# Kernel optimization log

Measured on AMD Instinct MI355X. Metric: run time of the kernel, lower is better.

## Reference

```python
import jax, jax.numpy as jnp
import numpy as np

EMBED_DIM = 1024
NUM_HEADS = 16
HEAD_DIM = EMBED_DIM // NUM_HEADS


def setup_inputs() -> dict:
    key = jax.random.key(0)
    k1, k2, k3, k4, k5 = jax.random.split(key, 5)
    B, S, D = 1, 4096, EMBED_DIM
    scale = 0.02
    return {
        "input": jax.random.normal(k1, (B, S, D), dtype=jnp.float32),
        "Wqkv": jax.random.normal(k2, (D, 3 * D), dtype=jnp.float32) * scale,
        "bqkv": jax.random.normal(k3, (3 * D,), dtype=jnp.float32) * scale,
        "Wo": jax.random.normal(k4, (D, D), dtype=jnp.float32) * scale,
        "bo": jax.random.normal(k5, (D,), dtype=jnp.float32) * scale,
    }


def reference(input, Wqkv, bqkv, Wo, bo):
    B, S, D = input.shape
    H, Hd = NUM_HEADS, HEAD_DIM
    qkv = input @ Wqkv + bqkv                        # [B, S, 3D]
    qkv = qkv.reshape(B, S, 3, H, Hd)
    qkv = jnp.transpose(qkv, (2, 0, 3, 1, 4))        # [3, B, H, S, Hd]
    q, k, v = qkv[0], qkv[1], qkv[2]
    scores = jnp.einsum("bhsd,bhtd->bhst", q, k) / (Hd ** 0.5)  # [B,H,S,S]
    causal = jnp.tril(jnp.ones((S, S), dtype=bool))[None, None]
    scores = jnp.where(causal, scores, -jnp.inf)
    attn = jax.nn.softmax(scores, axis=-1)
    out = jnp.einsum("bhst,bhtd->bhsd", attn, v)     # [B,H,S,Hd]
    out = jnp.transpose(out, (0, 2, 1, 3)).reshape(B, S, D)
    return out @ Wo + bo
```

## Files before the change

### kernel.cpp

```cpp
#include <hip/hip_runtime.h>

typedef __bf16 bf16;
typedef __bf16 bf16x8 __attribute__((ext_vector_type(8)));
typedef float f32x4 __attribute__((ext_vector_type(4)));
typedef float f32x16 __attribute__((ext_vector_type(16)));
typedef unsigned u32x2 __attribute__((ext_vector_type(2)));

#define MFMA16(a, b, c) __builtin_amdgcn_mfma_f32_16x16x32_bf16((a), (b), (c), 0, 0, 0)
#define MFMA32(a, b, c) __builtin_amdgcn_mfma_f32_32x32x16_bf16((a), (b), (c), 0, 0, 0)

typedef const __attribute__((address_space(1))) uint32_t glb_u32;
typedef __attribute__((address_space(3))) uint32_t lds_u32;
#define GLOAD16(gp, lp) __builtin_amdgcn_global_load_lds((glb_u32*)(gp), (lds_u32*)(lp), 16, 0, 0)

__global__ __launch_bounds__(256) void k_convX(const float* __restrict__ in, bf16* __restrict__ out) {
    size_t i = ((size_t)blockIdx.x * 256 + threadIdx.x) * 8;
    float4 a = *(const float4*)(in + i);
    float4 b = *(const float4*)(in + i + 4);
    bf16 e[8];
    e[0] = (bf16)a.x; e[1] = (bf16)a.y; e[2] = (bf16)a.z; e[3] = (bf16)a.w;
    e[4] = (bf16)b.x; e[5] = (bf16)b.y; e[6] = (bf16)b.z; e[7] = (bf16)b.w;
    uint4 u; __builtin_memcpy(&u, e, 16);
    *(uint4*)(out + i) = u;
}

__global__ __launch_bounds__(256) void k_tconv(const float* __restrict__ in, bf16* __restrict__ out,
                                               int R, int C) {
    __shared__ float tile[64][65];
    int bx = blockIdx.x, by = blockIdx.y;
    int t = threadIdx.x;
    for (int i = 0; i < 16; ++i) {
        int e = i * 256 + t; int r = e >> 6, c = e & 63;
        tile[r][c] = in[(size_t)(by * 64 + r) * C + bx * 64 + c];
    }
    __syncthreads();
    for (int i = 0; i < 16; ++i) {
        int e = i * 256 + t; int r = e >> 6, c = e & 63;
        out[(size_t)(bx * 64 + r) * R + by * 64 + c] = (bf16)tile[c][r];
    }
}

__device__ __forceinline__ void gemm128_core(const bf16* __restrict__ A, const bf16* __restrict__ Bt,
                                             int r0, int c0, int Kd, char* As, char* Bs,
                                             f32x4 (&acc)[4][4]) {
    int t = threadIdx.x, l = t & 63, w = t >> 6;
    int g = l >> 4, li = l & 15;
    int wr = w >> 1, wc = w & 1;
    for (int k0 = 0; k0 < Kd; k0 += 64) {
        __syncthreads();
        #pragma unroll
        for (int i = 0; i < 4; ++i) {
            int slot = i * 256 + t;
            int row = slot >> 3;
            int ch  = (slot & 7) ^ (row & 7);
            int base = (i * 256 + w * 64) * 16;
            GLOAD16(A  + (size_t)(r0 + row) * Kd + k0 + ch * 8, As + base);
            GLOAD16(Bt + (size_t)(c0 + row) * Kd + k0 + ch * 8, Bs + base);
        }
        __syncthreads();
        __builtin_amdgcn_s_setprio(1);
        #pragma unroll
        for (int kk = 0; kk < 2; ++kk) {
            bf16x8 af[4], bfr[4];
            #pragma unroll
            for (int m = 0; m < 4; ++m) {
                int row = wr * 64 + m * 16 + li;
                af[m] = *(const bf16x8*)(As + ((row * 128 + kk * 64 + g * 16) ^ ((row & 7) << 4)));
            }
            #pragma unroll
            for (int n = 0; n < 4; ++n) {
                int row = wc * 64 + n * 16 + li;
                bfr[n] = *(const bf16x8*)(Bs + ((row * 128 + kk * 64 + g * 16) ^ ((row & 7) << 4)));
            }
            #pragma unroll
            for (int m = 0; m < 4; ++m)
                #pragma unroll
                for (int n = 0; n < 4; ++n)
                    acc[m][n] = MFMA16(af[m], bfr[n], acc[m][n]);
        }
        __builtin_amdgcn_s_setprio(0);
    }
}

__global__ __launch_bounds__(256) void k_gemm_qkv(const bf16* __restrict__ Xb, const bf16* __restrict__ WqkvT,
                                                  const float* __restrict__ bqkv,
                                                  bf16* __restrict__ Q, bf16* __restrict__ Kfr,
                                                  bf16* __restrict__ Vfr) {
    __shared__ __align__(16) char As[16384];
    __shared__ __align__(16) char Bs[16384];
    int r0 = blockIdx.y * 128, c0 = blockIdx.x * 128;
    f32x4 acc[4][4] = {};
    gemm128_core(Xb, WqkvT, r0, c0, 1024, As, Bs, acc);
    int t = threadIdx.x, l = t & 63, w = t >> 6;
    int g = l >> 4, li = l & 15;
    int wr = w >> 1, wc = w & 1;
    int colbase = c0 + wc * 64;
    int sec = colbase >> 10;
    int head = (colbase & 1023) >> 6;
    if (sec == 0) {
        const float scale = 0.125f * 1.44269504f;
        #pragma unroll
        for (int m = 0; m < 4; ++m)
            #pragma unroll
            for (int n = 0; n < 4; ++n) {
                int hd = n * 16 + li;
                float bias = bqkv[colbase + hd];
                #pragma unroll
                for (int r = 0; r < 4; ++r) {
                    int row = r0 + wr * 64 + m * 16 + g * 4 + r;
                    Q[(size_t)(head * 4096 + row) * 64 + hd] = (bf16)((acc[m][n][r] + bias) * scale);
                }
            }
    } else if (sec == 1) {
        bf16* dstK = Kfr + (size_t)head * 262144;
        #pragma unroll
        for (int m = 0; m < 4; ++m) {
            int tbase = r0 + wr * 64 + m * 16 + g * 4;
            size_t tpart = (size_t)(tbase >> 5) * 2048 + (size_t)(tbase & 31) * 8;
            #pragma unroll
            for (int n = 0; n < 4; ++n) {
                int hd = n * 16 + li;
                float bias = bqkv[colbase + hd];
                size_t A0 = tpart + (size_t)(hd >> 4) * 512 + (size_t)((hd >> 3) & 1) * 256 + (hd & 7);
                #pragma unroll
                for (int r = 0; r < 4; ++r)
                    dstK[A0 + (size_t)r * 8] = (bf16)(acc[m][n][r] + bias);
            }
        }
    } else {
        bf16* dstV = Vfr + (size_t)head * 262144;
        #pragma unroll
        for (int m = 0; m < 4; ++m) {
            int tbase = r0 + wr * 64 + m * 16 + g * 4;
            size_t tpart = (size_t)(tbase >> 5) * 2048 + (size_t)((tbase >> 4) & 1) * 512
                         + (size_t)((tbase >> 3) & 1) * 256 + (tbase & 7);
            #pragma unroll
            for (int n = 0; n < 4; ++n) {
                int hd = n * 16 + li;
                float bias = bqkv[colbase + hd];
                size_t A0 = tpart + (size_t)(hd >> 5) * 1024 + (size_t)(hd & 31) * 8;
                bf16 e4[4];
                #pragma unroll
                for (int r = 0; r < 4; ++r) e4[r] = (bf16)(acc[m][n][r] + bias);
                unsigned long long pk; __builtin_memcpy(&pk, e4, 8);
                *(unsigned long long*)(dstV + A0) = pk;
            }
        }
    }
}

__global__ __launch_bounds__(256) void k_gemm_out(const bf16* __restrict__ Ob, const bf16* __restrict__ WoT,
                                                  const float* __restrict__ bo, float* __restrict__ out) {
    __shared__ __align__(16) char As[16384];
    __shared__ __align__(16) char Bs[8192];
    int r0 = blockIdx.y * 128, c0 = blockIdx.x * 64;
    int t = threadIdx.x, l = t & 63, w = t >> 6;
    int g = l >> 4, li = l & 15;
    f32x4 acc[2][4] = {};
    for (int k0 = 0; k0 < 1024; k0 += 64) {
        __syncthreads();
        #pragma unroll
        for (int i = 0; i < 4; ++i) {
            int slot = i * 256 + t;
            int row = slot >> 3;
            int ch  = (slot & 7) ^ (row & 7);
            int base = (i * 256 + w * 64) * 16;
            GLOAD16(Ob + (size_t)(r0 + row) * 1024 + k0 + ch * 8, As + base);
        }
        #pragma unroll
        for (int i = 0; i < 2; ++i) {
            int slot = i * 256 + t;
            int row = slot >> 3;
            int ch  = (slot & 7) ^ (row & 7);
            int base = (i * 256 + w * 64) * 16;
            GLOAD16(WoT + (size_t)(c0 + row) * 1024 + k0 + ch * 8, Bs + base);
        }
        __syncthreads();
        __builtin_amdgcn_s_setprio(1);
        #pragma unroll
        for (int kk = 0; kk < 2; ++kk) {
            bf16x8 af[2], bfr[4];
            #pragma unroll
            for (int m = 0; m < 2; ++m) {
                int row = w * 32 + m * 16 + li;
                af[m] = *(const bf16x8*)(As + ((row * 128 + kk * 64 + g * 16) ^ ((row & 7) << 4)));
            }
            #pragma unroll
            for (int n = 0; n < 4; ++n) {
                int row = n * 16 + li;
                bfr[n] = *(const bf16x8*)(Bs + ((row * 128 + kk * 64 + g * 16) ^ ((row & 7) << 4)));
            }
            #pragma unroll
            for (int m = 0; m < 2; ++m)
                #pragma unroll
                for (int n = 0; n < 4; ++n)
                    acc[m][n] = MFMA16(af[m], bfr[n], acc[m][n]);
        }
        __builtin_amdgcn_s_setprio(0);
    }
    #pragma unroll
    for (int m = 0; m < 2; ++m)
        #pragma unroll
        for (int n = 0; n < 4; ++n) {
            int col = c0 + n * 16 + li;
            float bias = bo[col];
            #pragma unroll
            for (int r = 0; r < 4; ++r) {
                int row = r0 + w * 32 + m * 16 + g * 4 + r;
                out[(size_t)row * 1024 + col] = acc[m][n][r] + bias;
            }
        }
}

__device__ __forceinline__ unsigned pkbf(float a, float b) {
    bf16 h0 = (bf16)a, h1 = (bf16)b;
    unsigned short u0, u1;
    __builtin_memcpy(&u0, &h0, 2); __builtin_memcpy(&u1, &h1, 2);
    return (unsigned)u0 | ((unsigned)u1 << 16);
}

__global__ __launch_bounds__(128) void k_attn(const bf16* __restrict__ Q, const uint4* __restrict__ Kfr,
                                              const uint4* __restrict__ Vfr, bf16* __restrict__ O) {
    __shared__ float Op[32][64];
    __shared__ float Ml[2][32];
    int bid = blockIdx.x;
    int h = bid & 15;
    int u = bid >> 4;
    int jj = (u < 64) ? u : 191 - u;
    int w = threadIdx.x >> 6;
    int l = threadIdx.x & 63;
    int lc = l & 31, hi = l >> 5;
    int hi4 = hi * 4, hi8 = hi * 8;
    const bf16* Qh = Q + (size_t)h * 4096 * 64;
    const uint4* Kh = Kfr + (size_t)h * 32768;
    const uint4* Vh = Vfr + (size_t)h * 32768;
    int nt = jj + 1;
    int hA = (nt + 1) >> 1;
    int tb = w ? hA : 0;
    int te = w ? nt : hA;

    f32x16 oacc[2] = {};
    float m = -1e30f, lsum = 0.f;
    uint4 kA[4], vA[4], kB[4], vB[4];
    bf16x8 qf[4];
    #pragma unroll
    for (int kst = 0; kst < 4; ++kst)
        qf[kst] = *(const bf16x8*)(Qh + (size_t)(jj * 32 + lc) * 64 + kst * 16 + hi8);

    auto compute = [&](int tt, uint4 (&kf)[4], uint4 (&vf)[4]) {
        f32x16 sacc = {};
        __builtin_amdgcn_s_setprio(1);
        #pragma unroll
        for (int kst = 0; kst < 4; ++kst) {
            bf16x8 kk; __builtin_memcpy(&kk, &kf[kst], 16);
            sacc = MFMA32(kk, qf[kst], sacc);
        }
        __builtin_amdgcn_s_setprio(0);
        if (tt == jj) {
            #pragma unroll
            for (int r = 0; r < 16; ++r) {
                int tloc = (r & 3) + 8 * (r >> 2) + hi4;
                if (tloc > lc) sacc[r] = -1e30f;
            }
        }
        float t8[8];
        #pragma unroll
        for (int r = 0; r < 8; ++r) t8[r] = fmaxf(sacc[r], sacc[r + 8]);
        float ta = fmaxf(fmaxf(t8[0], t8[1]), t8[2]);
        float tb3 = fmaxf(fmaxf(t8[3], t8[4]), t8[5]);
        float tc = fmaxf(t8[6], t8[7]);
        float pm = fmaxf(fmaxf(ta, tb3), tc);
        pm = fmaxf(pm, __shfl_xor(pm, 32));
        if (!__all(pm - m <= 8.0f)) {
            float mn = fmaxf(m, pm);
            float al = exp2f(m - mn);
            #pragma unroll
            for (int r = 0; r < 16; ++r) {
                int ql = (r & 3) + 8 * (r >> 2) + hi4;
                float alb = __shfl(al, ql);
                oacc[0][r] *= alb;
                oacc[1][r] *= alb;
            }
            lsum *= al;
            m = mn;
        }
        float pv[16];
        float rs0 = 0.f, rs1 = 0.f;
        #pragma unroll
        for (int r = 0; r < 8; ++r) {
            pv[r]     = exp2f(sacc[r] - m);     rs0 += pv[r];
            pv[r + 8] = exp2f(sacc[r + 8] - m); rs1 += pv[r + 8];
        }
        lsum += rs0 + rs1;
        #pragma unroll
        for (int ks = 0; ks < 2; ++ks) {
            int b = ks * 8;
            unsigned a0 = pkbf(pv[b + 0], pv[b + 1]), a1 = pkbf(pv[b + 2], pv[b + 3]);
            unsigned b0 = pkbf(pv[b + 4], pv[b + 5]), b1 = pkbf(pv[b + 6], pv[b + 7]);
            u32x2 r0 = __builtin_amdgcn_permlane32_swap(a0, b0, false, false);
            u32x2 r1 = __builtin_amdgcn_permlane32_swap(a1, b1, false, false);
            unsigned wsq[4] = { r0[0], r1[0], r0[1], r1[1] };
            bf16x8 pa; __builtin_memcpy(&pa, wsq, 16);
            __builtin_amdgcn_s_setprio(1);
            #pragma unroll
            for (int jt = 0; jt < 2; ++jt) {
                bf16x8 vv; __builtin_memcpy(&vv, &vf[jt * 2 + ks], 16);
                oacc[jt] = MFMA32(pa, vv, oacc[jt]);
            }
            __builtin_amdgcn_s_setprio(0);
        }
    };

    if (te > tb) {
        #pragma unroll
        for (int i = 0; i < 4; ++i) {
            kA[i] = Kh[(size_t)tb * 256 + i * 64 + l];
            vA[i] = Vh[(size_t)tb * 256 + i * 64 + l];
        }
        int i = tb;
        for (; i + 2 <= te; i += 2) {
            const uint4* Kn = Kh + (size_t)(i + 1) * 256;
            const uint4* Vn = Vh + (size_t)(i + 1) * 256;
            #pragma unroll
            for (int q = 0; q < 4; ++q) { kB[q] = Kn[q * 64 + l]; vB[q] = Vn[q * 64 + l]; }
            compute(i, kA, vA);
            if (i + 2 < te) {
                const uint4* K2 = Kh + (size_t)(i + 2) * 256;
                const uint4* V2 = Vh + (size_t)(i + 2) * 256;
                #pragma unroll
                for (int q = 0; q < 4; ++q) { kA[q] = K2[q * 64 + l]; vA[q] = V2[q * 64 + l]; }
            }
            compute(i + 1, kB, vB);
        }
        if ((te - tb) & 1) compute(te - 1, kA, vA);
    }
    lsum += __shfl_xor(lsum, 32);

    if (w == 1) {
        #pragma unroll
        for (int r = 0; r < 16; ++r) {
            int ql = (r & 3) + 8 * (r >> 2) + hi4;
            Op[ql][lc]      = oacc[0][r];
            Op[ql][32 + lc] = oacc[1][r];
        }
        if (hi == 0) { Ml[0][lc] = m; Ml[1][lc] = lsum; }
    }
    __syncthreads();
    if (w == 0) {
        float mo = Ml[0][lc], lo = Ml[1][lc];
        float mm = fmaxf(m, mo);
        float alr = exp2f(m - mm), alo = exp2f(mo - mm);
        float lf = lsum * alr + lo * alo;
        float inv = 1.0f / lf;
        float fr = alr * inv, fo = alo * inv;
        int q0 = jj * 32;
        #pragma unroll
        for (int r = 0; r < 16; ++r) {
            int ql = (r & 3) + 8 * (r >> 2) + hi4;
            float frb = __shfl(fr, ql), fob = __shfl(fo, ql);
            float o0 = oacc[0][r] * frb + Op[ql][lc]      * fob;
            float o1 = oacc[1][r] * frb + Op[ql][32 + lc] * fob;
            int row = q0 + ql;
            O[(size_t)row * 1024 + h * 64 + lc]      = (bf16)o0;
            O[(size_t)row * 1024 + h * 64 + 32 + lc] = (bf16)o1;
        }
    }
}

extern "C" void kernel_launch(void* const* d_in, const int* in_sizes, int n_in,
                              void* d_out, int out_size, void* d_ws, size_t ws_size,
                              hipStream_t stream) {
    const float* X    = (const float*)d_in[0];
    const float* Wqkv = (const float*)d_in[1];
    const float* bqkv = (const float*)d_in[2];
    const float* Wo   = (const float*)d_in[3];
    const float* bo   = (const float*)d_in[4];
    float* out = (float*)d_out;

    char* ws = (char*)d_ws;
    const size_t MB = 1024 * 1024;
    bf16*  Xb    = (bf16*)(ws);
    bf16*  WqkvT = (bf16*)(ws + 8  * MB);
    bf16*  WoT   = (bf16*)(ws + 14 * MB);
    bf16*  Qb    = (bf16*)(ws + 16 * MB);
    uint4* Kfr   = (uint4*)(ws + 40 * MB);
    uint4* Vfr   = (uint4*)(ws + 48 * MB);
    bf16*  Ob    = Xb;

    k_convX<<<2048, 256, 0, stream>>>(X, Xb);
    k_tconv<<<dim3(48, 16), 256, 0, stream>>>(Wqkv, WqkvT, 1024, 3072);
    k_tconv<<<dim3(16, 16), 256, 0, stream>>>(Wo, WoT, 1024, 1024);
    k_gemm_qkv<<<dim3(24, 32), 256, 0, stream>>>(Xb, WqkvT, bqkv, Qb, (bf16*)Kfr, (bf16*)Vfr);
    k_attn<<<2048, 128, 0, stream>>>(Qb, Kfr, Vfr, Ob);
    k_gemm_out<<<dim3(16, 32), 256, 0, stream>>>(Ob, WoT, bo, out);
}
```

Before: 151.3 us.

## Merge prep kernels into one launch and remap GEMM blocks per XCD

The three preprocessing kernels (X conversion and the two weight transposes) are merged into a single launch that dispatches on block index. This removes two kernel launches and their gaps. The QKV and output GEMMs now use a 1D grid with a remap (bid&7)*N + bid>>3, which places contiguous tiles on the same XCD to improve L2 reuse under round-robin XCD dispatch. The risk is that the merged prep kernel has uneven per-block work, and the remap may not suit the cache layout.

```diff
diff --git a/kernel.cpp b/kernel.cpp
--- a/kernel.cpp
+++ b/kernel.cpp
@@ -13,22 +13,31 @@
 typedef __attribute__((address_space(3))) uint32_t lds_u32;
 #define GLOAD16(gp, lp) __builtin_amdgcn_global_load_lds((glb_u32*)(gp), (lds_u32*)(lp), 16, 0, 0)
 
-__global__ __launch_bounds__(256) void k_convX(const float* __restrict__ in, bf16* __restrict__ out) {
-    size_t i = ((size_t)blockIdx.x * 256 + threadIdx.x) * 8;
-    float4 a = *(const float4*)(in + i);
-    float4 b = *(const float4*)(in + i + 4);
-    bf16 e[8];
-    e[0] = (bf16)a.x; e[1] = (bf16)a.y; e[2] = (bf16)a.z; e[3] = (bf16)a.w;
-    e[4] = (bf16)b.x; e[5] = (bf16)b.y; e[6] = (bf16)b.z; e[7] = (bf16)b.w;
-    uint4 u; __builtin_memcpy(&u, e, 16);
-    *(uint4*)(out + i) = u;
-}
-
-__global__ __launch_bounds__(256) void k_tconv(const float* __restrict__ in, bf16* __restrict__ out,
-                                               int R, int C) {
+__global__ __launch_bounds__(256) void k_prep(const float* __restrict__ X, bf16* __restrict__ Xb,
+                                              const float* __restrict__ Wqkv, bf16* __restrict__ WqkvT,
+                                              const float* __restrict__ Wo, bf16* __restrict__ WoT) {
     __shared__ float tile[64][65];
-    int bx = blockIdx.x, by = blockIdx.y;
+    int bid = blockIdx.x;
     int t = threadIdx.x;
+    if (bid < 2048) {
+        size_t i = ((size_t)bid * 256 + t) * 8;
+        float4 a = *(const float4*)(X + i);
+        float4 b = *(const float4*)(X + i + 4);
+        bf16 e[8];
+        e[0] = (bf16)a.x; e[1] = (bf16)a.y; e[2] = (bf16)a.z; e[3] = (bf16)a.w;
+        e[4] = (bf16)b.x; e[5] = (bf16)b.y; e[6] = (bf16)b.z; e[7] = (bf16)b.w;
+        uint4 u; __builtin_memcpy(&u, e, 16);
+        *(uint4*)(Xb + i) = u;
+        return;
+    }
+    const float* in; bf16* out; int R, C, bx, by;
+    if (bid < 2816) {
+        in = Wqkv; out = WqkvT; R = 1024; C = 3072;
+        int b = bid - 2048; bx = b % 48; by = b / 48;
+    } else {
+        in = Wo; out = WoT; R = 1024; C = 1024;
+        int b = bid - 2816; bx = b & 15; by = b >> 4;
+    }
     for (int i = 0; i < 16; ++i) {
         int e = i * 256 + t; int r = e >> 6, c = e & 63;
         tile[r][c] = in[(size_t)(by * 64 + r) * C + bx * 64 + c];
@@ -88,7 +97,10 @@
                                                   bf16* __restrict__ Vfr) {
     __shared__ __align__(16) char As[16384];
     __shared__ __align__(16) char Bs[16384];
-    int r0 = blockIdx.y * 128, c0 = blockIdx.x * 128;
+    int bid = blockIdx.x;
+    int Lg = (bid & 7) * 96 + (bid >> 3);
+    int bx = Lg % 24, by = Lg / 24;
+    int r0 = by * 128, c0 = bx * 128;
     f32x4 acc[4][4] = {};
     gemm128_core(Xb, WqkvT, r0, c0, 1024, As, Bs, acc);
     int t = threadIdx.x, l = t & 63, w = t >> 6;
@@ -153,7 +165,10 @@
                                                   const float* __restrict__ bo, float* __restrict__ out) {
     __shared__ __align__(16) char As[16384];
     __shared__ __align__(16) char Bs[8192];
-    int r0 = blockIdx.y * 128, c0 = blockIdx.x * 64;
+    int bid = blockIdx.x;
+    int Lg = (bid & 7) * 64 + (bid >> 3);
+    int bx = Lg & 15, by = Lg >> 4;
+    int r0 = by * 128, c0 = bx * 64;
     int t = threadIdx.x, l = t & 63, w = t >> 6;
     int g = l >> 4, li = l & 15;
     f32x4 acc[2][4] = {};
@@ -387,10 +402,8 @@
     uint4* Vfr   = (uint4*)(ws + 48 * MB);
     bf16*  Ob    = Xb;
 
-    k_convX<<<2048, 256, 0, stream>>>(X, Xb);
-    k_tconv<<<dim3(48, 16), 256, 0, stream>>>(Wqkv, WqkvT, 1024, 3072);
-    k_tconv<<<dim3(16, 16), 256, 0, stream>>>(Wo, WoT, 1024, 1024);
-    k_gemm_qkv<<<dim3(24, 32), 256, 0, stream>>>(Xb, WqkvT, bqkv, Qb, (bf16*)Kfr, (bf16*)Vfr);
+    k_prep<<<3072, 256, 0, stream>>>(X, Xb, Wqkv, WqkvT, Wo, WoT);
+    k_gemm_qkv<<<768, 256, 0, stream>>>(Xb, WqkvT, bqkv, Qb, (bf16*)Kfr, (bf16*)Vfr);
     k_attn<<<2048, 128, 0, stream>>>(Qb, Kfr, Vfr, Ob);
-    k_gemm_out<<<dim3(16, 32), 256, 0, stream>>>(Ob, WoT, bo, out);
-}
+    k_gemm_out<<<512, 256, 0, stream>>>(Ob, WoT, bo, out);
+}
```

Measured after the change: 147.8 us. 2.3% less time.
